# Optimization experiments

Hardware: AMD Instinct MI355X
Metric: run time of the kernel (lower is better)

The kernel has to match this reference:

```python
import jax, jax.numpy as jnp
import numpy as np


def setup_inputs() -> dict:
    key = jax.random.key(0)
    k1, k2 = jax.random.split(key)
    B, S, H, D = 4, 2048, 12, 64
    v = jax.random.normal(k1, (B, S, H, D), dtype=jnp.float32)
    # learned per-head positional weights, sorted ascending along last dim
    # (mirrors torch.sort(torch.randn(H, S), dim=-1)[0])
    w = jnp.sort(jax.random.normal(k2, (H, S), dtype=jnp.float32), axis=-1)
    return {"v": v, "w": w}


def reference(v, w):
    # PositionalBias._naive
    # v: [B, S, H, D]; w: [H, S_max]
    B, S, H, D = v.shape
    seq_len = S - 2  # v[:, 1:-1] is the non-special-token span
    w_ = w[:, :seq_len]  # [H, seq_len]
    # _construct_bias builds bias[h, l, j] = w[h, |l - j|] (symmetric Toeplitz)
    pos = jnp.arange(seq_len)
    idx = jnp.abs(pos[:, None] - pos[None, :])  # [seq_len, seq_len]
    bias = w_[:, idx]  # [H, seq_len, seq_len]
    # zero-pad one row/col on each side -> [H, S, S]
    bias = jnp.pad(bias, ((0, 0), (1, 1), (1, 1)))
    # z_pb: [1, S, H]
    z_pb = jnp.sum(bias, axis=-1).T[None, :, :]
    # pbv: [B, S, H, D]
    pbv = jnp.einsum('nlhd,hlj->njhd', v, bias)
    return (pbv, z_pb)
```

## Files before the change

### kernel.cpp

```cpp
#include <hip/hip_runtime.h>
#include <hip/hip_bf16.h>


typedef short short8 __attribute__((ext_vector_type(8)));
typedef float floatx4 __attribute__((ext_vector_type(4)));

typedef const __attribute__((address_space(1))) void gvoid_t;
typedef __attribute__((address_space(3))) void lvoid_t;

__device__ __forceinline__ unsigned short f2bf(float f) {
  union { __hip_bfloat16 b; unsigned short u; } cv;
  cv.b = __float2bfloat16(f);
  return cv.u;
}

__global__ __launch_bounds__(256) void transpose_kernel(const float* __restrict__ v,
                                                        unsigned short* __restrict__ vb) {
  __shared__ float tile[64][65];
  const int lt = blockIdx.x;
  const int h  = blockIdx.y;
  const int n  = blockIdx.z;
  const int tid = threadIdx.x;
  const int l0 = lt * 64;
  {
    const int d  = tid & 63;
    const int r0 = tid >> 6;
    #pragma unroll
    for (int rr = 0; rr < 16; ++rr) {
      int ll = r0 * 16 + rr;
      tile[ll][d] = v[(((size_t)n * 2048 + (l0 + ll)) * 12 + h) * 64 + d];
    }
  }
  __syncthreads();
  {
    const int d = tid >> 2;
    const int q = tid & 3;
    unsigned short buf[16] __attribute__((aligned(16)));
    #pragma unroll
    for (int jj = 0; jj < 16; ++jj) {
      int l = l0 + q * 16 + jj;
      float f = tile[q * 16 + jj][d];
      buf[jj] = (l == 0 || l == 2047) ? (unsigned short)0 : f2bf(f);
    }
    unsigned short* dst = vb + ((size_t)h * 256 + n * 64 + d) * 2048 + l0 + q * 16;
    *(uint4*)dst       = *(const uint4*)&buf[0];
    *(uint4*)(dst + 8) = *(const uint4*)&buf[8];
  }
}

__global__ __launch_bounds__(256) void zpb_kernel(const float* __restrict__ w,
                                                  float* __restrict__ zout) {
  __shared__ float wv[2048];
  __shared__ float part[256];
  __shared__ float pfx[2048];
  const int h = blockIdx.x;
  const int tid = threadIdx.x;
  const float* wh = w + (size_t)h * 2048;
  for (int i = tid; i < 2048; i += 256) wv[i] = (i < 2046) ? wh[i] : 0.f;
  __syncthreads();
  float s = 0.f;
  #pragma unroll
  for (int k = 0; k < 8; ++k) s += wv[tid * 8 + k];
  part[tid] = s;
  __syncthreads();
  if (tid == 0) {
    float run = 0.f;
    for (int t = 0; t < 256; ++t) { float tmp = part[t]; part[t] = run; run += tmp; }
  }
  __syncthreads();
  float run = part[tid];
  #pragma unroll
  for (int k = 0; k < 8; ++k) { run += wv[tid * 8 + k]; pfx[tid * 8 + k] = run; }
  __syncthreads();
  for (int i = tid; i < 2046; i += 256) {
    float z = pfx[i] + pfx[2045 - i] - wv[0];
    zout[(size_t)(i + 1) * 12 + h] = z;
  }
  if (tid == 0) { zout[h] = 0.f; zout[(size_t)2047 * 12 + h] = 0.f; }
}

__global__ __launch_bounds__(256, 2) void gemm_kernel(const float* __restrict__ w,
                                                      const unsigned short* __restrict__ vb,
                                                      float* __restrict__ out) {
  __shared__ short we[4112];
  __shared__ short vt[2][128][32];

  const int jt  = blockIdx.x;
  const int ndt = blockIdx.y;
  const int h   = blockIdx.z;
  const int tid = threadIdx.x;
  const int lane = tid & 63;
  const int wid  = tid >> 6;
  const int wm = wid >> 1, wn = wid & 1;
  const int lm = lane & 15, quad = lane >> 4;

  const float* wh = w + (size_t)h * 2048;
  for (int i = tid; i < 4112; i += 256) {
    int t = i - 2055;
    int a = t < 0 ? -t : t;
    float val = (a <= 2045) ? wh[a] : 0.f;
    we[i] = (short)f2bf(val);
  }
  __syncthreads();

  const int nd0 = ndt * 128;
  const int jw  = jt * 128 + wm * 64;
  const int ndw = nd0 + wn * 64;
  const unsigned short* vbp = vb + (size_t)h * 256 * 2048;

  floatx4 acc[4][4];
  #pragma unroll
  for (int ma = 0; ma < 4; ++ma)
    #pragma unroll
    for (int na = 0; na < 4; ++na)
      acc[ma][na] = (floatx4){0.f, 0.f, 0.f, 0.f};

  auto load_af = [&](int q, int l0) -> short8 {
    int base = jw + (q - 2) * 16 + lm - (l0 + quad * 8) + 2055;
    short8 r;
    #pragma unroll
    for (int i = 0; i < 8; ++i) r[i] = we[base - i];
    return r;
  };

  short8 a4 = load_af(4, 0);
  short8 a5 = load_af(5, 0);

  #pragma unroll 1
  for (int l0 = 0; l0 < 2048; l0 += 64) {
    #pragma unroll
    for (int s = 0; s < 2; ++s) {
      #pragma unroll
      for (int u = 0; u < 2; ++u) {
        int e  = wid * 2 + u;
        int r0 = e * 16;
        int grow = nd0 + r0 + (lane >> 2);
        int gcol = l0 + s * 32 + (lane & 3) * 8;
        const unsigned short* g = vbp + (size_t)grow * 2048 + gcol;
        __builtin_amdgcn_global_load_lds((gvoid_t*)g, (lvoid_t*)&vt[s][r0][0], 16, 0, 0);
      }
    }
    asm volatile("s_waitcnt vmcnt(0)" ::: "memory");
    __syncthreads();

    short8 afr[6];
    #pragma unroll
    for (int q = 0; q < 4; ++q) afr[q] = load_af(q, l0);
    afr[4] = a4; afr[5] = a5;
    a4 = afr[0]; a5 = afr[1];

    #pragma unroll
    for (int kc = 0; kc < 2; ++kc) {
      short8 bfr[4];
      #pragma unroll
      for (int na = 0; na < 4; ++na)
        bfr[na] = *(const short8*)&vt[kc][wn * 64 + na * 16 + lm][quad * 8];
      #pragma unroll
      for (int ma = 0; ma < 4; ++ma) {
        short8 af = afr[kc ? ma : ma + 2];
        #pragma unroll
        for (int na = 0; na < 4; ++na)
          acc[ma][na] = __builtin_amdgcn_mfma_f32_16x16x32_bf16(af, bfr[na], acc[ma][na], 0, 0, 0);
      }
    }
    __syncthreads();
  }

  #pragma unroll
  for (int ma = 0; ma < 4; ++ma) {
    #pragma unroll
    for (int na = 0; na < 4; ++na) {
      floatx4 c = acc[ma][na];
      int ndv = ndw + na * 16 + lm;
      int n = ndv >> 6, d = ndv & 63;
      #pragma unroll
      for (int r = 0; r < 4; ++r) {
        int j = jw + ma * 16 + quad * 4 + r;
        float val = (j == 0 || j == 2047) ? 0.f : c[r];
        out[(size_t)n * 1572864 + (size_t)j * 768 + h * 64 + d] = val;
      }
    }
  }
}

extern "C" void kernel_launch(void* const* d_in, const int* in_sizes, int n_in,
                              void* d_out, int out_size, void* d_ws, size_t ws_size,
                              hipStream_t stream) {
  const float* v = (const float*)d_in[0];
  const float* w = (const float*)d_in[1];
  float* out = (float*)d_out;
  unsigned short* vb = (unsigned short*)d_ws;

  transpose_kernel<<<dim3(32, 12, 4), 256, 0, stream>>>(v, vb);
  zpb_kernel<<<dim3(12), 256, 0, stream>>>(w, out + 6291456);
  gemm_kernel<<<dim3(16, 2, 12), 256, 0, stream>>>(w, vb, out);
}
```

Before: 131.0 us.

## Store Toeplitz weights as 8 shifted copies for vector LDS A-fragment loads

```diff
diff --git a/kernel.cpp b/kernel.cpp
--- a/kernel.cpp
+++ b/kernel.cpp
@@ -51,26 +51,33 @@
 __global__ __launch_bounds__(256) void zpb_kernel(const float* __restrict__ w,
                                                   float* __restrict__ zout) {
   __shared__ float wv[2048];
-  __shared__ float part[256];
   __shared__ float pfx[2048];
+  __shared__ float wsum[4];
   const int h = blockIdx.x;
   const int tid = threadIdx.x;
   const float* wh = w + (size_t)h * 2048;
   for (int i = tid; i < 2048; i += 256) wv[i] = (i < 2046) ? wh[i] : 0.f;
   __syncthreads();
-  float s = 0.f;
-  #pragma unroll
-  for (int k = 0; k < 8; ++k) s += wv[tid * 8 + k];
-  part[tid] = s;
-  __syncthreads();
-  if (tid == 0) {
-    float run = 0.f;
-    for (int t = 0; t < 256; ++t) { float tmp = part[t]; part[t] = run; run += tmp; }
-  }
-  __syncthreads();
-  float run = part[tid];
-  #pragma unroll
-  for (int k = 0; k < 8; ++k) { run += wv[tid * 8 + k]; pfx[tid * 8 + k] = run; }
+  const int base = tid * 8;
+  float run0 = 0.f;
+  #pragma unroll
+  for (int k = 0; k < 8; ++k) run0 += wv[base + k];
+  float x = run0;
+  #pragma unroll
+  for (int d = 1; d < 64; d <<= 1) {
+    float y = __shfl_up(x, d);
+    if ((tid & 63) >= d) x += y;
+  }
+  if ((tid & 63) == 63) wsum[tid >> 6] = x;
+  __syncthreads();
+  const int wid = tid >> 6;
+  float woff = 0.f;
+  #pragma unroll
+  for (int u = 0; u < 3; ++u) { float t = wsum[u]; if (u < wid) woff += t; }
+  float excl = x + woff - run0;
+  float pr = excl;
+  #pragma unroll
+  for (int k = 0; k < 8; ++k) { pr += wv[base + k]; pfx[base + k] = pr; }
   __syncthreads();
   for (int i = tid; i < 2046; i += 256) {
     float z = pfx[i] + pfx[2045 - i] - wv[0];
@@ -82,8 +89,8 @@
 __global__ __launch_bounds__(256, 2) void gemm_kernel(const float* __restrict__ w,
                                                       const unsigned short* __restrict__ vb,
                                                       float* __restrict__ out) {
-  __shared__ short we[4112];
-  __shared__ short vt[2][128][32];
+  __shared__ __attribute__((aligned(16))) short Tls[8 * 2184];
+  __shared__ __attribute__((aligned(16))) short vt[2][128][32];
 
   const int jt  = blockIdx.x;
   const int ndt = blockIdx.y;
@@ -93,18 +100,25 @@
   const int wid  = tid >> 6;
   const int wm = wid >> 1, wn = wid & 1;
   const int lm = lane & 15, quad = lane >> 4;
+  const int jb = jt * 128;
 
   const float* wh = w + (size_t)h * 2048;
-  for (int i = tid; i < 4112; i += 256) {
-    int t = i - 2055;
-    int a = t < 0 ? -t : t;
-    float val = (a <= 2045) ? wh[a] : 0.f;
-    we[i] = (short)f2bf(val);
+  for (int g = tid; g < 8 * 273; g += 256) {
+    int c  = g / 273;
+    int p8 = (g - c * 273) * 8;
+    unsigned short buf[8] __attribute__((aligned(16)));
+    #pragma unroll
+    for (int i = 0; i < 8; ++i) {
+      int t = 127 + jb - (p8 + i) - c;
+      int a = t < 0 ? -t : t;
+      buf[i] = (a <= 2045) ? f2bf(wh[a]) : (unsigned short)0;
+    }
+    *(short8*)&Tls[c * 2184 + p8] = *(const short8*)buf;
   }
   __syncthreads();
 
   const int nd0 = ndt * 128;
-  const int jw  = jt * 128 + wm * 64;
+  const int jw  = jb + wm * 64;
   const int ndw = nd0 + wn * 64;
   const unsigned short* vbp = vb + (size_t)h * 256 * 2048;
 
@@ -115,16 +129,15 @@
     for (int na = 0; na < 4; ++na)
       acc[ma][na] = (floatx4){0.f, 0.f, 0.f, 0.f};
 
-  auto load_af = [&](int q, int l0) -> short8 {
-    int base = jw + (q - 2) * 16 + lm - (l0 + quad * 8) + 2055;
-    short8 r;
-    #pragma unroll
-    for (int i = 0; i < 8; ++i) r[i] = we[base - i];
-    return r;
+  const int pbase = 127 + quad * 8 - wm * 64 - lm;
+  auto load_af = [&](int g16, int l0) -> short8 {
+    int p0 = l0 + g16 + pbase;
+    int c  = p0 & 7;
+    return *(const short8*)&Tls[c * 2184 + (p0 - c)];
   };
 
-  short8 a4 = load_af(4, 0);
-  short8 a5 = load_af(5, 0);
+  short8 a4 = load_af(-48, 0);
+  short8 a5 = load_af(-32, 0);
 
   #pragma unroll 1
   for (int l0 = 0; l0 < 2048; l0 += 64) {
@@ -144,10 +157,12 @@
     __syncthreads();
 
     short8 afr[6];
-    #pragma unroll
-    for (int q = 0; q < 4; ++q) afr[q] = load_af(q, l0);
-    afr[4] = a4; afr[5] = a5;
-    a4 = afr[0]; a5 = afr[1];
+    afr[0] = a4; afr[1] = a5;
+    afr[2] = load_af(-16, l0);
+    afr[3] = load_af(0,   l0);
+    afr[4] = load_af(16,  l0);
+    afr[5] = load_af(32,  l0);
+    a4 = afr[4]; a5 = afr[5];
 
     #pragma unroll
     for (int kc = 0; kc < 2; ++kc) {
@@ -157,7 +172,7 @@
         bfr[na] = *(const short8*)&vt[kc][wn * 64 + na * 16 + lm][quad * 8];
       #pragma unroll
       for (int ma = 0; ma < 4; ++ma) {
-        short8 af = afr[kc ? ma : ma + 2];
+        short8 af = afr[(kc ? 5 : 3) - ma];
         #pragma unroll
         for (int na = 0; na < 4; ++na)
           acc[ma][na] = __builtin_amdgcn_mfma_f32_16x16x32_bf16(af, bfr[na], acc[ma][na], 0, 0, 0);
```

Result: faster. 126.5 us (-3.5%).
